# Optimization experiments

Measured on AMD Instinct MI355X. Metric: run time of the kernel, lower is better.

The kernel has to match this reference:

```python
import jax, jax.numpy as jnp
import numpy as np

TK_W = 0.6
G_W = 0.4
HN_W = 0.5
HN_K = 2
EPS_CLIP = 1e-4


def setup_inputs() -> dict:
    key = jax.random.key(0)
    B, C = 4096, 8192
    k1, k2, k3, k4, k5 = jax.random.split(key, 5)
    # probabilities strictly inside (0,1) so BCE logs are finite
    tk_scores = jnp.clip(jax.random.uniform(k1, (B, C), jnp.float32), EPS_CLIP, 1.0 - EPS_CLIP)
    g_scores = jnp.clip(jax.random.uniform(k2, (B, C), jnp.float32), EPS_CLIP, 1.0 - EPS_CLIP)
    # binary 0/1 float targets (sparse positives)
    tk_targets = (jax.random.uniform(k3, (B, C), jnp.float32) > 0.9).astype(jnp.float32)
    g_targets = (jax.random.uniform(k4, (B, C), jnp.float32) > 0.9).astype(jnp.float32)
    confidences = jax.random.uniform(k5, (B,), jnp.float32)
    return {"tk_scores": tk_scores, "g_scores": g_scores,
            "tk_targets": tk_targets, "g_targets": g_targets,
            "confidences": confidences}


def _bce(p, t):
    # BCELoss(reduction='none'): -(t*log(p) + (1-t)*log(1-p))
    return -(t * jnp.log(p) + (1.0 - t) * jnp.log1p(-p))


def _hard_negative_mask(preds, targets, k):
    # top (3k) predictions per row, then first k whose target < 0.5 (in descending-score order)
    B, C = preds.shape
    top_k = max(1, min(C, k * 3))
    _, idx = jax.lax.top_k(preds, top_k)                       # [B, top_k], sorted desc
    tgt_at = jnp.take_along_axis(targets, idx, axis=1) < 0.5   # [B, top_k] is-negative
    cum = jnp.cumsum(tgt_at.astype(jnp.int32), axis=1)
    sel = tgt_at & (cum <= k)                                  # first k negatives only
    rows = jnp.arange(B)[:, None]
    return jnp.zeros_like(preds).at[rows, idx].add(sel.astype(preds.dtype))


def _directional_loss(scores, targets, conf_w):
    loss_mat = _bce(scores, targets)
    pos = (loss_mat * conf_w).mean()
    mask = _hard_negative_mask(jax.lax.stop_gradient(scores), targets, HN_K)
    msum = mask.sum()
    # if mask sum is 0 the numerator is 0 too, so unconditional form matches torch branch
    neg = (loss_mat * mask).sum() / (msum + 1e-8)
    return pos + HN_W * neg


def reference(tk_scores, g_scores, tk_targets, g_targets, confidences):
    conf_w = confidences[:, None]
    tk_loss = _directional_loss(tk_scores, tk_targets, conf_w)
    g_loss = _directional_loss(g_scores, g_targets, conf_w)
    total = TK_W * tk_loss + G_W * g_loss
    return total, tk_loss, g_loss
```

## Files before the change

kernel.cpp:

```cpp
#include <hip/hip_runtime.h>

#define NB 4096
#define NC 8192

__global__ __launch_bounds__(256) void row_stats(
    const float* __restrict__ tk_s, const float* __restrict__ g_s,
    const float* __restrict__ tk_t, const float* __restrict__ g_t,
    const float* __restrict__ conf, float* __restrict__ ws) {
  const int lane = threadIdx.x & 63;
  const int wave = threadIdx.x >> 6;
  const int row  = (blockIdx.x << 2) + wave;
  const int mat  = blockIdx.y;

  const float4* S4 = reinterpret_cast<const float4*>(
      (mat ? g_s : tk_s) + (size_t)row * NC);
  const float4* T4 = reinterpret_cast<const float4*>(
      (mat ? g_t : tk_t) + (size_t)row * NC);

  unsigned lk0=0,lk1=0,lk2=0,lk3=0,lk4=0,lk5=0;
  unsigned lp0=0,lp1=0,lp2=0,lp3=0,lp4=0,lp5=0;
  float bl2 = 0.0f;
  unsigned tseed;

  float4 s0 = S4[lane],      t0 = T4[lane];
  float4 s1 = S4[64 + lane], t1 = T4[64 + lane];
  {
    float m4 = fmaxf(fmaxf(s0.x, s0.y), fmaxf(s0.z, s0.w));
    m4 = fmaxf(m4, __shfl_xor(m4, 1));
    m4 = fmaxf(m4, __shfl_xor(m4, 2));
    m4 = fmaxf(m4, __shfl_xor(m4, 4));
    m4 = fminf(m4, __shfl_xor(m4, 8));
    m4 = fminf(m4, __shfl_xor(m4, 16));
    m4 = fminf(m4, __shfl_xor(m4, 32));
    tseed = __float_as_uint(m4) - 1u;
  }

#define INS(KJ, PJ) { if (ck_ > KJ) { unsigned tk_ = KJ, tp_ = PJ;        \
    KJ = ck_; PJ = cp_; ck_ = tk_; cp_ = tp_; } }
#define TRY(KE, QE, CE) { unsigned key_ = __builtin_amdgcn_readlane(KE, l_); \
    if (key_ > lk5) {                                                     \
      unsigned ck_ = key_;                                                \
      unsigned cp_ = ((unsigned)(CE) << 1) |                              \
                     (unsigned)((QE >> l_) & 1ull);                       \
      INS(lk0, lp0) INS(lk1, lp1) INS(lk2, lp2)                           \
      INS(lk3, lp3) INS(lk4, lp4) INS(lk5, lp5)                           \
    } }

  auto process = [&](float4 sv, float4 tv, int i) {
    float b0 = (sv.x + tv.x) - 1.0f;
    float b1 = (sv.y + tv.y) - 1.0f;
    float b2 = (sv.z + tv.z) - 1.0f;
    float b3 = (sv.w + tv.w) - 1.0f;
    float pr = (fabsf(b0) * fabsf(b1)) * (fabsf(b2) * fabsf(b3));
    bl2 += __log2f(pr);
    float m4 = fmaxf(fmaxf(sv.x, sv.y), fmaxf(sv.z, sv.w));
    float thrf = __uint_as_float(lk5 > tseed ? lk5 : tseed);
    unsigned long long m_ = __ballot(m4 > thrf);
    if (m_) {
      unsigned long long q0 = __ballot(tv.x > 0.5f);
      unsigned long long q1 = __ballot(tv.y > 0.5f);
      unsigned long long q2 = __ballot(tv.z > 0.5f);
      unsigned long long q3 = __ballot(tv.w > 0.5f);
      unsigned kx = __float_as_uint(sv.x), ky = __float_as_uint(sv.y);
      unsigned kz = __float_as_uint(sv.z), kw = __float_as_uint(sv.w);
      do {
        int l_ = __ffsll(m_) - 1;
        m_ &= m_ - 1;
        unsigned c_ = (unsigned)(((i) * 64 + l_) * 4);
        TRY(kx, q0, c_)
        TRY(ky, q1, c_ + 1)
        TRY(kz, q2, c_ + 2)
        TRY(kw, q3, c_ + 3)
      } while (m_);
    }
  };

  #pragma unroll 2
  for (int i = 0; i < 30; ++i) {
    float4 sn = S4[(i + 2) * 64 + lane];
    float4 tn = T4[(i + 2) * 64 + lane];
    process(s0, t0, i);
    s0 = s1; t0 = t1; s1 = sn; t1 = tn;
  }
  process(s0, t0, 30);
  process(s1, t1, 31);
#undef TRY
#undef INS

  #pragma unroll
  for (int off = 32; off > 0; off >>= 1) bl2 += __shfl_xor(bl2, off);

  if (lane == 0) {
    float nsum = 0.0f; int cnt = 0;
#define SELN(ki, pi) { if (((pi) & 1u) == 0u && cnt < 2) {                \
      nsum += -__logf(1.0f - __uint_as_float(ki)); cnt++; } }
    SELN(lk0, lp0) SELN(lk1, lp1) SELN(lk2, lp2)
    SELN(lk3, lp3) SELN(lk4, lp4) SELN(lk5, lp5)
#undef SELN
    const int base = mat * NB + row;
    const float ln2 = 0.6931471805599453f;
    ws[base]          = conf[row] * (-bl2 * ln2);
    ws[2 * NB + base] = nsum;
    ws[4 * NB + base] = (float)cnt;
  }
}

__global__ __launch_bounds__(256) void finalize_loss(
    const float* __restrict__ ws, float* __restrict__ out) {
  __shared__ float red[6][256];
  const int t = threadIdx.x;
  float a[6] = {0.f, 0.f, 0.f, 0.f, 0.f, 0.f};
  for (int r = t; r < NB; r += 256) {
    #pragma unroll
    for (int j = 0; j < 6; ++j) a[j] += ws[j * NB + r];
  }
  #pragma unroll
  for (int j = 0; j < 6; ++j) red[j][t] = a[j];
  __syncthreads();
  for (int s = 128; s > 0; s >>= 1) {
    if (t < s) {
      #pragma unroll
      for (int j = 0; j < 6; ++j) red[j][t] += red[j][t + s];
    }
    __syncthreads();
  }
  if (t == 0) {
    const float inv = 1.0f / ((float)NB * (float)NC);
    float tk = red[0][0] * inv + 0.5f * (red[2][0] / (red[4][0] + 1e-8f));
    float g  = red[1][0] * inv + 0.5f * (red[3][0] / (red[5][0] + 1e-8f));
    out[0] = 0.6f * tk + 0.4f * g;
    out[1] = tk;
    out[2] = g;
  }
}

extern "C" void kernel_launch(void* const* d_in, const int* in_sizes, int n_in,
                              void* d_out, int out_size, void* d_ws, size_t ws_size,
                              hipStream_t stream) {
  const float* tk_s = (const float*)d_in[0];
  const float* g_s  = (const float*)d_in[1];
  const float* tk_t = (const float*)d_in[2];
  const float* g_t  = (const float*)d_in[3];
  const float* conf = (const float*)d_in[4];
  float* ws  = (float*)d_ws;
  float* out = (float*)d_out;

  dim3 grid(NB / 4, 2);
  row_stats<<<grid, 256, 0, stream>>>(tk_s, g_s, tk_t, g_t, conf, ws);
  finalize_loss<<<1, 256, 0, stream>>>(ws, out);
}
```

Before: 109.7 us.

## Fuse final reduction into row kernel via last-block ticket, two rows per wave

```diff
diff --git a/kernel.cpp b/kernel.cpp
--- a/kernel.cpp
+++ b/kernel.cpp
@@ -2,20 +2,14 @@
 
 #define NB 4096
 #define NC 8192
+#define RPW 2
+#define NBLK ((NB / (4 * RPW)) * 2)
 
-__global__ __launch_bounds__(256) void row_stats(
-    const float* __restrict__ tk_s, const float* __restrict__ g_s,
-    const float* __restrict__ tk_t, const float* __restrict__ g_t,
-    const float* __restrict__ conf, float* __restrict__ ws) {
-  const int lane = threadIdx.x & 63;
-  const int wave = threadIdx.x >> 6;
-  const int row  = (blockIdx.x << 2) + wave;
-  const int mat  = blockIdx.y;
-
-  const float4* S4 = reinterpret_cast<const float4*>(
-      (mat ? g_s : tk_s) + (size_t)row * NC);
-  const float4* T4 = reinterpret_cast<const float4*>(
-      (mat ? g_t : tk_t) + (size_t)row * NC);
+__device__ __forceinline__ void row_body(
+    const float* __restrict__ S, const float* __restrict__ T,
+    int lane, float conf_r, float* __restrict__ ws, int base) {
+  const float4* S4 = reinterpret_cast<const float4*>(S);
+  const float4* T4 = reinterpret_cast<const float4*>(T);
 
   unsigned lk0=0,lk1=0,lk2=0,lk3=0,lk4=0,lk5=0;
   unsigned lp0=0,lp1=0,lp2=0,lp3=0,lp4=0,lp5=0;
@@ -37,7 +31,8 @@
 
 #define INS(KJ, PJ) { if (ck_ > KJ) { unsigned tk_ = KJ, tp_ = PJ;        \
     KJ = ck_; PJ = cp_; ck_ = tk_; cp_ = tp_; } }
-#define TRY(KE, QE, CE) { unsigned key_ = __builtin_amdgcn_readlane(KE, l_); \
+#define TRY(KE, QE, CE) { unsigned key_ =                                 \
+      (unsigned)__builtin_amdgcn_readlane((int)(KE), l_);                 \
     if (key_ > lk5) {                                                     \
       unsigned ck_ = key_;                                                \
       unsigned cp_ = ((unsigned)(CE) << 1) |                              \
@@ -97,16 +92,41 @@
     SELN(lk0, lp0) SELN(lk1, lp1) SELN(lk2, lp2)
     SELN(lk3, lp3) SELN(lk4, lp4) SELN(lk5, lp5)
 #undef SELN
-    const int base = mat * NB + row;
     const float ln2 = 0.6931471805599453f;
-    ws[base]          = conf[row] * (-bl2 * ln2);
+    ws[base]          = conf_r * (-bl2 * ln2);
     ws[2 * NB + base] = nsum;
     ws[4 * NB + base] = (float)cnt;
   }
 }
 
-__global__ __launch_bounds__(256) void finalize_loss(
-    const float* __restrict__ ws, float* __restrict__ out) {
+__global__ __launch_bounds__(256) void row_stats(
+    const float* __restrict__ tk_s, const float* __restrict__ g_s,
+    const float* __restrict__ tk_t, const float* __restrict__ g_t,
+    const float* __restrict__ conf, float* __restrict__ ws,
+    unsigned* __restrict__ counter, float* __restrict__ out) {
+  const int lane = threadIdx.x & 63;
+  const int wave = threadIdx.x >> 6;
+  const int mat  = blockIdx.y;
+  const int row0 = ((blockIdx.x << 2) + wave) * RPW;
+
+  const float* Sb = mat ? g_s : tk_s;
+  const float* Tb = mat ? g_t : tk_t;
+
+  #pragma unroll
+  for (int r = 0; r < RPW; ++r) {
+    const int row = row0 + r;
+    row_body(Sb + (size_t)row * NC, Tb + (size_t)row * NC,
+             lane, conf[row], ws, mat * NB + row);
+  }
+
+  __threadfence();
+  __syncthreads();
+  __shared__ unsigned ticket;
+  if (threadIdx.x == 0) ticket = atomicAdd(counter, 1u);
+  __syncthreads();
+  if (ticket != NBLK - 1) return;
+
+  __threadfence();
   __shared__ float red[6][256];
   const int t = threadIdx.x;
   float a[6] = {0.f, 0.f, 0.f, 0.f, 0.f, 0.f};
@@ -143,9 +163,11 @@
   const float* g_t  = (const float*)d_in[3];
   const float* conf = (const float*)d_in[4];
   float* ws  = (float*)d_ws;
+  unsigned* counter = (unsigned*)((char*)d_ws + 6 * NB * sizeof(float));
   float* out = (float*)d_out;
 
-  dim3 grid(NB / 4, 2);
-  row_stats<<<grid, 256, 0, stream>>>(tk_s, g_s, tk_t, g_t, conf, ws);
-  finalize_loss<<<1, 256, 0, stream>>>(ws, out);
+  hipMemsetAsync(counter, 0, sizeof(unsigned), stream);
+  dim3 grid(NB / (4 * RPW), 2);
+  row_stats<<<grid, 256, 0, stream>>>(tk_s, g_s, tk_t, g_t, conf, ws,
+                                      counter, out);
 }
```

Result: slower. 305.7 us (+178.8%).

## Split each row across two waves and merge top-k via shared memory

Applied to the files above, without the earlier changes.

```diff
diff --git a/kernel.cpp b/kernel.cpp
--- a/kernel.cpp
+++ b/kernel.cpp
@@ -2,20 +2,21 @@
 
 #define NB 4096
 #define NC 8192
+#define HALF (NC / 2)
 
-__global__ __launch_bounds__(256) void row_stats(
+__global__ __launch_bounds__(128) void row_stats(
     const float* __restrict__ tk_s, const float* __restrict__ g_s,
     const float* __restrict__ tk_t, const float* __restrict__ g_t,
     const float* __restrict__ conf, float* __restrict__ ws) {
   const int lane = threadIdx.x & 63;
-  const int wave = threadIdx.x >> 6;
-  const int row  = (blockIdx.x << 2) + wave;
+  const int half = threadIdx.x >> 6;
+  const int row  = blockIdx.x;
   const int mat  = blockIdx.y;
 
-  const float4* S4 = reinterpret_cast<const float4*>(
-      (mat ? g_s : tk_s) + (size_t)row * NC);
-  const float4* T4 = reinterpret_cast<const float4*>(
-      (mat ? g_t : tk_t) + (size_t)row * NC);
+  const float* Sb = (mat ? g_s : tk_s) + (size_t)row * NC + half * HALF;
+  const float* Tb = (mat ? g_t : tk_t) + (size_t)row * NC + half * HALF;
+  const float4* S4 = reinterpret_cast<const float4*>(Sb);
+  const float4* T4 = reinterpret_cast<const float4*>(Tb);
 
   unsigned lk0=0,lk1=0,lk2=0,lk3=0,lk4=0,lk5=0;
   unsigned lp0=0,lp1=0,lp2=0,lp3=0,lp4=0,lp5=0;
@@ -37,7 +38,8 @@
 
 #define INS(KJ, PJ) { if (ck_ > KJ) { unsigned tk_ = KJ, tp_ = PJ;        \
     KJ = ck_; PJ = cp_; ck_ = tk_; cp_ = tp_; } }
-#define TRY(KE, QE, CE) { unsigned key_ = __builtin_amdgcn_readlane(KE, l_); \
+#define TRY(KE, QE, CE) { unsigned key_ =                                 \
+      (unsigned)__builtin_amdgcn_readlane((int)(KE), l_);                 \
     if (key_ > lk5) {                                                     \
       unsigned ck_ = key_;                                                \
       unsigned cp_ = ((unsigned)(CE) << 1) |                              \
@@ -76,58 +78,84 @@
   };
 
   #pragma unroll 2
-  for (int i = 0; i < 30; ++i) {
+  for (int i = 0; i < 14; ++i) {
     float4 sn = S4[(i + 2) * 64 + lane];
     float4 tn = T4[(i + 2) * 64 + lane];
     process(s0, t0, i);
     s0 = s1; t0 = t1; s1 = sn; t1 = tn;
   }
-  process(s0, t0, 30);
-  process(s1, t1, 31);
+  process(s0, t0, 14);
+  process(s1, t1, 15);
 #undef TRY
 #undef INS
 
   #pragma unroll
   for (int off = 32; off > 0; off >>= 1) bl2 += __shfl_xor(bl2, off);
 
+  __shared__ unsigned kk[2][6], pp[2][6];
+  __shared__ float bl[2];
   if (lane == 0) {
-    float nsum = 0.0f; int cnt = 0;
-#define SELN(ki, pi) { if (((pi) & 1u) == 0u && cnt < 2) {                \
-      nsum += -__logf(1.0f - __uint_as_float(ki)); cnt++; } }
-    SELN(lk0, lp0) SELN(lk1, lp1) SELN(lk2, lp2)
-    SELN(lk3, lp3) SELN(lk4, lp4) SELN(lk5, lp5)
-#undef SELN
+    kk[half][0]=lk0; kk[half][1]=lk1; kk[half][2]=lk2;
+    kk[half][3]=lk3; kk[half][4]=lk4; kk[half][5]=lk5;
+    pp[half][0]=lp0; pp[half][1]=lp1; pp[half][2]=lp2;
+    pp[half][3]=lp3; pp[half][4]=lp4; pp[half][5]=lp5;
+    bl[half] = bl2;
+  }
+  __syncthreads();
+  if (threadIdx.x == 0) {
+    float nsum = 0.0f; int cnt = 0, ia = 0, ib = 0;
+    #pragma unroll
+    for (int n = 0; n < 6; ++n) {
+      bool takeA = (ib >= 6) || (ia < 6 && kk[0][ia] >= kk[1][ib]);
+      unsigned key = takeA ? kk[0][ia] : kk[1][ib];
+      unsigned pay = takeA ? pp[0][ia] : pp[1][ib];
+      if (takeA) ++ia; else ++ib;
+      if ((pay & 1u) == 0u && cnt < 2) {
+        nsum += -__logf(1.0f - __uint_as_float(key));
+        ++cnt;
+      }
+    }
     const int base = mat * NB + row;
     const float ln2 = 0.6931471805599453f;
-    ws[base]          = conf[row] * (-bl2 * ln2);
+    ws[base]          = conf[row] * (-(bl[0] + bl[1]) * ln2);
     ws[2 * NB + base] = nsum;
     ws[4 * NB + base] = (float)cnt;
   }
 }
 
-__global__ __launch_bounds__(256) void finalize_loss(
+__global__ __launch_bounds__(1024) void finalize_loss(
     const float* __restrict__ ws, float* __restrict__ out) {
-  __shared__ float red[6][256];
+  __shared__ float red[6][16];
   const int t = threadIdx.x;
-  float a[6] = {0.f, 0.f, 0.f, 0.f, 0.f, 0.f};
-  for (int r = t; r < NB; r += 256) {
-    #pragma unroll
-    for (int j = 0; j < 6; ++j) a[j] += ws[j * NB + r];
+  const int lane = t & 63, w = t >> 6;
+  const float4* W4 = reinterpret_cast<const float4*>(ws);
+  float a[6];
+  #pragma unroll
+  for (int j = 0; j < 6; ++j) {
+    float4 v = W4[j * (NB / 4) + t];
+    a[j] = (v.x + v.y) + (v.z + v.w);
   }
   #pragma unroll
-  for (int j = 0; j < 6; ++j) red[j][t] = a[j];
+  for (int j = 0; j < 6; ++j) {
+    #pragma unroll
+    for (int off = 32; off > 0; off >>= 1) a[j] += __shfl_xor(a[j], off);
+  }
+  if (lane == 0) {
+    #pragma unroll
+    for (int j = 0; j < 6; ++j) red[j][w] = a[j];
+  }
   __syncthreads();
-  for (int s = 128; s > 0; s >>= 1) {
-    if (t < s) {
-      #pragma unroll
-      for (int j = 0; j < 6; ++j) red[j][t] += red[j][t + s];
+  if (t == 0) {
+    float s[6];
+    #pragma unroll
+    for (int j = 0; j < 6; ++j) {
+      float acc = 0.0f;
+      for (int u = 0; u < 16; ++u) acc += red[j][u];
+      s[j] = acc;
     }
-    __syncthreads();
-  }
-  if (t == 0) {
     const float inv = 1.0f / ((float)NB * (float)NC);
-    float tk = red[0][0] * inv + 0.5f * (red[2][0] / (red[4][0] + 1e-8f));
-    float g  = red[1][0] * inv + 0.5f * (red[3][0] / (red[5][0] + 1e-8f));
+    float tk = s[0] * inv + 0.5f * (s[2] / (s[4] + 1e-8f));
+    float g  = s[1] * inv + 0.5f * (s[3] / (s[5] + 1e-8f));
     out[0] = 0.6f * tk + 0.4f * g;
     out[1] = tk;
     out[2] = g;
@@ -145,7 +173,7 @@
   float* ws  = (float*)d_ws;
   float* out = (float*)d_out;
 
-  dim3 grid(NB / 4, 2);
-  row_stats<<<grid, 256, 0, stream>>>(tk_s, g_s, tk_t, g_t, conf, ws);
-  finalize_loss<<<1, 256, 0, stream>>>(ws, out);
+  dim3 grid(NB, 2);
+  row_stats<<<grid, 128, 0, stream>>>(tk_s, g_s, tk_t, g_t, conf, ws);
+  finalize_loss<<<1, 1024, 0, stream>>>(ws, out);
 }
```

After: 111.4 us. No clear change (+1.6%).
